# Kernel tuning notes

Measured on AMD Instinct MI355X. Metric: run time of the kernel, lower is better.

The kernel has to match this reference:

```python
import jax, jax.numpy as jnp
import numpy as np

D_MODEL = 768
H = 12
D_FF = 3072
EPS = 1e-6


def _layernorm(x, alpha, bias):
    # torch.std default is Bessel-corrected (ddof=1); denom is (std + eps)
    mean = jnp.mean(x, axis=-1, keepdims=True)
    var = jnp.sum((x - mean) ** 2, axis=-1, keepdims=True) / (x.shape[-1] - 1)
    std = jnp.sqrt(var)
    return alpha * (x - mean) / (std + EPS) + bias


def _linear(x, w, b):
    # torch nn.Linear: y = x @ W.T + b, W is [out, in]
    return jnp.einsum('...i,oi->...o', x, w) + b


def setup_inputs() -> dict:
    key = jax.random.key(0)
    ks = jax.random.split(key, 16)
    B, S = 8, 1024
    sc = 1.0 / np.sqrt(D_MODEL)
    inp = {
        'x': jax.random.normal(ks[0], (B, S, D_MODEL), dtype=jnp.float32),
        'mask': jax.random.randint(ks[1], (B, 1, 1, S), 0, 2, dtype=jnp.int32),
        'wq': jax.random.normal(ks[2], (D_MODEL, D_MODEL), dtype=jnp.float32) * sc,
        'bq': jnp.zeros((D_MODEL,), jnp.float32),
        'wk': jax.random.normal(ks[3], (D_MODEL, D_MODEL), dtype=jnp.float32) * sc,
        'bk': jnp.zeros((D_MODEL,), jnp.float32),
        'wv': jax.random.normal(ks[4], (D_MODEL, D_MODEL), dtype=jnp.float32) * sc,
        'bv': jnp.zeros((D_MODEL,), jnp.float32),
        'wo': jax.random.normal(ks[5], (D_MODEL, D_MODEL), dtype=jnp.float32) * sc,
        'bo': jnp.zeros((D_MODEL,), jnp.float32),
        'ln1_a': jnp.ones((D_MODEL,), jnp.float32),
        'ln1_b': jnp.zeros((D_MODEL,), jnp.float32),
        'ln2_a': jnp.ones((D_MODEL,), jnp.float32),
        'ln2_b': jnp.zeros((D_MODEL,), jnp.float32),
        'w1': jax.random.normal(ks[6], (D_FF, D_MODEL), dtype=jnp.float32) * sc,
        'b1': jnp.zeros((D_FF,), jnp.float32),
        'w2': jax.random.normal(ks[7], (D_MODEL, D_FF), dtype=jnp.float32) * (1.0 / np.sqrt(D_FF)),
        'b2': jnp.zeros((D_MODEL,), jnp.float32),
    }
    return inp


def reference(x, mask, wq, bq, wk, bk, wv, bv, wo, bo,
              ln1_a, ln1_b, ln2_a, ln2_b, w1, b1, w2, b2):
    B, S, _ = x.shape
    d_k = D_MODEL // H

    # --- residual 1: pre-LN self-attention (dropout identity at eval) ---
    xn = _layernorm(x, ln1_a, ln1_b)
    q = _linear(xn, wq, bq).reshape(B, S, H, d_k).transpose(0, 2, 1, 3)
    k = _linear(xn, wk, bk).reshape(B, S, H, d_k).transpose(0, 2, 1, 3)
    v = _linear(xn, wv, bv).reshape(B, S, H, d_k).transpose(0, 2, 1, 3)

    scores = jnp.einsum('bhqd,bhkd->bhqk', q, k) / jnp.sqrt(jnp.float32(d_k))
    # faithful quirk: masked positions set to 1e-9, NOT -inf
    scores = jnp.where(mask == 0, jnp.float32(1e-9), scores)
    attn = jax.nn.softmax(scores, axis=-1)
    ctx = jnp.einsum('bhqk,bhkd->bhqd', attn, v)
    ctx = ctx.transpose(0, 2, 1, 3).reshape(B, S, D_MODEL)
    x = x + _linear(ctx, wo, bo)

    # --- residual 2: pre-LN feed-forward ---
    xn = _layernorm(x, ln2_a, ln2_b)
    ff = _linear(jax.nn.relu(_linear(xn, w1, b1)), w2, b2)
    return x + ff
```

## Files before the change

### kernel.cpp

```cpp
#include <hip/hip_runtime.h>
#include <stdint.h>

#define D_MODEL 768
#define D_FF    3072
#define NH      12
#define DK      64
#define BB      8
#define SS      1024
#define NTOK    (BB*SS)
#define QST     2304

typedef float          f32x4  __attribute__((ext_vector_type(4)));
typedef __bf16         bf16x8 __attribute__((ext_vector_type(8)));
typedef unsigned short us8v   __attribute__((ext_vector_type(8)));
typedef unsigned short us4v   __attribute__((ext_vector_type(4)));

__device__ __forceinline__ unsigned short f2b(float f) {
  unsigned int u = __builtin_bit_cast(unsigned int, f);
  u = (u + 0x7fffu + ((u >> 16) & 1u)) >> 16;
  return (unsigned short)u;
}
__device__ __forceinline__ float b2f(unsigned short h) {
  unsigned int u = ((unsigned int)h) << 16;
  return __builtin_bit_cast(float, u);
}
__device__ __forceinline__ float exp2a(float x) {
  float r; asm("v_exp_f32 %0, %1" : "=v"(r) : "v"(x)); return r;
}
__device__ __forceinline__ unsigned int cvtpk(float lo, float hi) {
  unsigned int r;
  asm("v_cvt_pk_bf16_f32 %0, %1, %2" : "=v"(r) : "v"(lo), "v"(hi));
  return r;
}

#define N4TOT 1769472
__global__ __launch_bounds__(256) void cast6_kernel(
    const float* __restrict__ s0, const float* __restrict__ s1,
    const float* __restrict__ s2, const float* __restrict__ s3,
    const float* __restrict__ s4, const float* __restrict__ s5,
    unsigned short* __restrict__ d0, unsigned short* __restrict__ d1,
    unsigned short* __restrict__ d2, unsigned short* __restrict__ d3,
    unsigned short* __restrict__ d4, unsigned short* __restrict__ d5) {
  int i = blockIdx.x * 256 + threadIdx.x;
  if (i >= N4TOT) return;
  const float* src; unsigned short* dst; int off;
  if (i < 147456)       { src = s0; dst = d0; off = i; }
  else if (i < 294912)  { src = s1; dst = d1; off = i - 147456; }
  else if (i < 442368)  { src = s2; dst = d2; off = i - 294912; }
  else if (i < 589824)  { src = s3; dst = d3; off = i - 442368; }
  else if (i < 1179648) { src = s4; dst = d4; off = i - 589824; }
  else                  { src = s5; dst = d5; off = i - 1179648; }
  float4 f = ((const float4*)src)[off];
  us4v o; o.x = f2b(f.x); o.y = f2b(f.y); o.z = f2b(f.z); o.w = f2b(f.w);
  *(us4v*)(dst + (size_t)off * 4) = o;
}

__global__ __launch_bounds__(256) void ln_kernel(const float* __restrict__ x,
                                                 const float* __restrict__ ga,
                                                 const float* __restrict__ gb,
                                                 unsigned short* __restrict__ y) {
  int row = blockIdx.x;
  const float* xr = x + (size_t)row * D_MODEL;
  int t = threadIdx.x, w = t >> 6, l = t & 63;
  float v0 = xr[t], v1 = xr[t + 256], v2 = xr[t + 512];
  float s = v0 + v1 + v2;
  #pragma unroll
  for (int off = 32; off; off >>= 1) s += __shfl_xor(s, off);
  __shared__ float red[4];
  __shared__ float stats[2];
  if (l == 0) red[w] = s;
  __syncthreads();
  if (t == 0) stats[0] = (red[0] + red[1] + red[2] + red[3]) * (1.0f / 768.0f);
  __syncthreads();
  float mean = stats[0];
  float d0 = v0 - mean, d1 = v1 - mean, d2 = v2 - mean;
  float ss = d0 * d0 + d1 * d1 + d2 * d2;
  #pragma unroll
  for (int off = 32; off; off >>= 1) ss += __shfl_xor(ss, off);
  __syncthreads();
  if (l == 0) red[w] = ss;
  __syncthreads();
  if (t == 0) {
    float tot = red[0] + red[1] + red[2] + red[3];
    stats[1] = 1.0f / (sqrtf(tot * (1.0f / 767.0f)) + 1e-6f);
  }
  __syncthreads();
  float inv = stats[1];
  unsigned short* yr = y + (size_t)row * D_MODEL;
  yr[t]       = f2b(ga[t]       * (d0 * inv) + gb[t]);
  yr[t + 256] = f2b(ga[t + 256] * (d1 * inv) + gb[t + 256]);
  yr[t + 512] = f2b(ga[t + 512] * (d2 * inv) + gb[t + 512]);
}

#define GLDS(g, l) __builtin_amdgcn_global_load_lds( \
    (__attribute__((address_space(1))) const void*)(g), \
    (__attribute__((address_space(3))) void*)(l), 16, 0, 0)

template<int BN>
__global__ __launch_bounds__(256) void gemm_t(
    const unsigned short* __restrict__ A,
    const unsigned short* __restrict__ W,
    const float* __restrict__ biasA,
    const float* __restrict__ biasB,
    const float* __restrict__ biasC,
    int segw,
    const float* __restrict__ resid,
    float* __restrict__ outF,
    unsigned short* __restrict__ outB,
    int M, int N, int K, int relu) {
  constexpr int BK  = (BN == 128) ? 32 : 64;
  constexpr int WC  = (BN == 128) ? 2 : 1;
  constexpr int MF  = (BN == 128) ? 4 : 2;
  constexpr int NF  = 4;
  constexpr int ASZ = 128 * BK;
  constexpr int BSZ = BN * BK;
  __shared__ unsigned short As[2 * ASZ];
  __shared__ unsigned short Bs[2 * BSZ];
  int t = threadIdx.x;
  int w = t >> 6, l = t & 63;
  int brow = blockIdx.x * 128;
  int bcol = blockIdx.y * BN;
  int wr = (w / WC) * (MF * 16);
  int wc = (w % WC) * (NF * 16);

  const unsigned short *ga0, *ga1, *gb0, *gb1;
  if constexpr (BN == 128) {
    ga0 = A + (size_t)(brow + (t >> 2)) * K + (t & 3) * 8;
    ga1 = ga0 + (size_t)64 * K;
    gb0 = W + (size_t)(bcol + (t >> 2)) * K + (t & 3) * 8;
    gb1 = gb0 + (size_t)64 * K;
  } else {
    int r5 = t >> 3;
    int swz = (t & 7) ^ (r5 & 7);
    ga0 = A + (size_t)(brow + r5) * K + swz * 8;
    gb0 = W + (size_t)(bcol + r5) * K + swz * 8;
    ga1 = gb1 = nullptr;
  }

  f32x4 acc[MF][NF];
  #pragma unroll
  for (int m = 0; m < MF; m++)
    #pragma unroll
    for (int n = 0; n < NF; n++)
      acc[m][n] = (f32x4){0.f, 0.f, 0.f, 0.f};

  int arow = wr + (l & 15);
  int bcw  = wc + (l & 15);
  int g    = l >> 4;
  int kk   = g * 8;
  const int nt = K / BK;

  auto stage = [&](int ti, int buf) {
    int k0 = ti * BK;
    if constexpr (BN == 128) {
      GLDS(ga0 + k0, As + buf * ASZ + t * 8);
      GLDS(ga1 + k0, As + buf * ASZ + 2048 + t * 8);
      GLDS(gb0 + k0, Bs + buf * BSZ + t * 8);
      GLDS(gb1 + k0, Bs + buf * BSZ + 2048 + t * 8);
    } else {
      #pragma unroll
      for (int i = 0; i < 4; i++)
        GLDS(ga0 + k0 + (size_t)(32 * i) * K, As + buf * ASZ + i * 2048 + t * 8);
      #pragma unroll
      for (int i = 0; i < 2; i++)
        GLDS(gb0 + k0 + (size_t)(32 * i) * K, Bs + buf * BSZ + i * 2048 + t * 8);
    }
  };

  stage(0, 0);
  __syncthreads();

  int cb = 0;
  for (int ti = 0; ti < nt; ti++) {
    if (ti + 1 < nt) stage(ti + 1, cb ^ 1);
    #pragma unroll
    for (int h = 0; h < BK / 32; h++) {
      bf16x8 af[MF], bfv[NF];
      #pragma unroll
      for (int m = 0; m < MF; m++) {
        int aro = arow + m * 16;
        if constexpr (BN == 128)
          af[m] = *(const bf16x8*)(As + cb * ASZ + aro * 32 + kk);
        else
          af[m] = *(const bf16x8*)(As + cb * ASZ + aro * 64 +
                                   ((((h << 2) + g) ^ (l & 7)) << 3));
      }
      #pragma unroll
      for (int n = 0; n < NF; n++) {
        int bco = bcw + n * 16;
        if constexpr (BN == 128)
          bfv[n] = *(const bf16x8*)(Bs + cb * BSZ + bco * 32 + kk);
        else
          bfv[n] = *(const bf16x8*)(Bs + cb * BSZ + bco * 64 +
                                    ((((h << 2) + g) ^ (l & 7)) << 3));
      }
      #pragma unroll
      for (int m = 0; m < MF; m++)
        #pragma unroll
        for (int n = 0; n < NF; n++)
          acc[m][n] = __builtin_amdgcn_mfma_f32_16x16x32_bf16(af[m], bfv[n], acc[m][n], 0, 0, 0);
    }
    if (ti + 1 < nt) __syncthreads();
    cb ^= 1;
  }

  #pragma unroll
  for (int n = 0; n < NF; n++) {
    int col = bcol + wc + n * 16 + (l & 15);
    int seg = col / segw, off = col - seg * segw;
    const float* bp = (seg == 0) ? biasA : ((seg == 1) ? biasB : biasC);
    float bv = bp[off];
    #pragma unroll
    for (int m = 0; m < MF; m++) {
      int row0 = brow + wr + m * 16 + (l >> 4) * 4;
      #pragma unroll
      for (int r = 0; r < 4; r++) {
        int row = row0 + r;
        float vacc = acc[m][n][r] + bv;
        if (resid) vacc += resid[(size_t)row * N + col];
        if (relu)  vacc = fmaxf(vacc, 0.f);
        if (outF)  outF[(size_t)row * N + col] = vacc;
        if (outB)  outB[(size_t)row * N + col] = f2b(vacc);
      }
    }
  }
}

#define PPAD 72
#define KPAD 72
#define SM_C1 0.18033688011112043f

__global__ __launch_bounds__(256) void attn_mfma(
    const unsigned short* __restrict__ qkv,
    const int* __restrict__ mask,
    unsigned short* __restrict__ ctx) {
  int bh = blockIdx.x;
  int qt = blockIdx.y;
  int b = bh / NH, h = bh % NH;
  int t = threadIdx.x, w = t >> 6, l = t & 63;
  int ql = l & 15, g = l >> 4;

  const unsigned short* kp = qkv + 768 + h * DK;
  const unsigned short* vp = qkv + 1536 + h * DK;

  __shared__ unsigned short Ks[4096];
  __shared__ unsigned short Vt[64 * KPAD];
  __shared__ unsigned short Ps[128 * PPAD];
  __shared__ float mk01[64];
  __shared__ float lrw[4][2][16];

  int srow = t >> 3;
  int sblk = t & 7;
  int sb0  = sblk ^ (srow & 7);
  int sb1  = sblk ^ ((srow + 32) & 7);

  bf16x8 qf[2][2];
  {
    const unsigned short* qp = qkv + h * DK;
    size_t row0 = (size_t)(b * SS + qt * 128 + w * 32 + ql);
    #pragma unroll
    for (int s = 0; s < 2; s++)
      #pragma unroll
      for (int ks = 0; ks < 2; ks++)
        qf[s][ks] = *(const bf16x8*)(qp + (row0 + s * 16) * QST + ks * 32 + g * 8);
  }

  f32x4 acc_o[2][4];
  #pragma unroll
  for (int s = 0; s < 2; s++)
    #pragma unroll
    for (int nf = 0; nf < 4; nf++) acc_o[s][nf] = (f32x4){0.f, 0.f, 0.f, 0.f};
  float lrun[2] = {0.f, 0.f};

  for (int kt = 0; kt < 16; kt++) {
    size_t tok0 = (size_t)(b * SS + kt * 64);
    GLDS(kp + (tok0 + srow)      * QST + sb0 * 8, Ks + t * 8);
    GLDS(kp + (tok0 + srow + 32) * QST + sb1 * 8, Ks + 2048 + t * 8);
    {
      const unsigned short* vsrc = vp + (tok0 + l) * QST + w * 16;
      us8v v0 = *(const us8v*)vsrc;
      us8v v1 = *(const us8v*)(vsrc + 8);
      #pragma unroll
      for (int j = 0; j < 8; j++) {
        Vt[(w * 16 + j)     * KPAD + l] = v0[j];
        Vt[(w * 16 + 8 + j) * KPAD + l] = v1[j];
      }
    }
    if (t < 64) mk01[t] = mask[b * SS + kt * 64 + t] ? SM_C1 : 0.0f;
    __syncthreads();

    f32x4 sa[2][4];
    #pragma unroll
    for (int s = 0; s < 2; s++)
      #pragma unroll
      for (int kf = 0; kf < 4; kf++) sa[s][kf] = (f32x4){0.f, 0.f, 0.f, 0.f};
    #pragma unroll
    for (int ks = 0; ks < 2; ks++) {
      bf16x8 kfr[4];
      #pragma unroll
      for (int kf = 0; kf < 4; kf++) {
        int row = kf * 16 + ql;
        kfr[kf] = *(const bf16x8*)(Ks + row * 64 + ((g + 4 * ks) ^ (ql & 7)) * 8);
      }
      #pragma unroll
      for (int s = 0; s < 2; s++)
        #pragma unroll
        for (int kf = 0; kf < 4; kf++)
          sa[s][kf] = __builtin_amdgcn_mfma_f32_16x16x32_bf16(kfr[kf], qf[s][ks], sa[s][kf], 0, 0, 0);
    }

    float mv[16];
    #pragma unroll
    for (int kf = 0; kf < 4; kf++)
      #pragma unroll
      for (int r = 0; r < 4; r++)
        mv[kf * 4 + r] = mk01[kf * 16 + g * 4 + r];

    #pragma unroll
    for (int s = 0; s < 2; s++) {
      float pv[16];
      float rs = 0.f;
      #pragma unroll
      for (int i = 0; i < 16; i++) {
        pv[i] = exp2a(sa[s][i >> 2][i & 3] * mv[i]);
        rs += pv[i];
      }
      rs += __shfl_xor(rs, 16);
      rs += __shfl_xor(rs, 32);
      lrun[s] += rs;

      int prow = w * 32 + s * 16 + ql;
      #pragma unroll
      for (int kf = 0; kf < 4; kf++) {
        uint2 pk;
        pk.x = cvtpk(pv[kf * 4 + 0], pv[kf * 4 + 1]);
        pk.y = cvtpk(pv[kf * 4 + 2], pv[kf * 4 + 3]);
        *(uint2*)(Ps + prow * PPAD + kf * 16 + g * 4) = pk;
      }
    }

    #pragma unroll
    for (int ks = 0; ks < 2; ks++) {
      bf16x8 vfr[4];
      #pragma unroll
      for (int nf = 0; nf < 4; nf++)
        vfr[nf] = *(const bf16x8*)(Vt + (ql + nf * 16) * KPAD + g * 8 + ks * 32);
      #pragma unroll
      for (int s = 0; s < 2; s++) {
        bf16x8 pa = *(const bf16x8*)(Ps + (w * 32 + s * 16 + ql) * PPAD + g * 8 + ks * 32);
        #pragma unroll
        for (int nf = 0; nf < 4; nf++)
          acc_o[s][nf] = __builtin_amdgcn_mfma_f32_16x16x32_bf16(pa, vfr[nf], acc_o[s][nf], 0, 0, 0);
      }
    }
    __syncthreads();
  }

  #pragma unroll
  for (int s = 0; s < 2; s++)
    if (l < 16) lrw[w][s][l] = lrun[s];
  #pragma unroll
  for (int s = 0; s < 2; s++) {
    float li0 = 1.0f / lrw[w][s][g * 4 + 0], li1 = 1.0f / lrw[w][s][g * 4 + 1];
    float li2 = 1.0f / lrw[w][s][g * 4 + 2], li3 = 1.0f / lrw[w][s][g * 4 + 3];
    #pragma unroll
    for (int nf = 0; nf < 4; nf++) {
      #pragma unroll
      for (int r = 0; r < 4; r++) {
        float li = (r == 0) ? li0 : (r == 1) ? li1 : (r == 2) ? li2 : li3;
        int tok = b * SS + qt * 128 + w * 32 + s * 16 + g * 4 + r;
        ctx[(size_t)tok * D_MODEL + h * DK + nf * 16 + ql] = f2b(acc_o[s][nf][r] * li);
      }
    }
  }
}

extern "C" void kernel_launch(void* const* d_in, const int* in_sizes, int n_in,
                              void* d_out, int out_size, void* d_ws, size_t ws_size,
                              hipStream_t stream) {
  const float* x    = (const float*)d_in[0];
  const int*   mask = (const int*)d_in[1];
  const float* wq   = (const float*)d_in[2];
  const float* bq   = (const float*)d_in[3];
  const float* wk   = (const float*)d_in[4];
  const float* bk   = (const float*)d_in[5];
  const float* wv   = (const float*)d_in[6];
  const float* bv   = (const float*)d_in[7];
  const float* wo   = (const float*)d_in[8];
  const float* bo   = (const float*)d_in[9];
  const float* ln1a = (const float*)d_in[10];
  const float* ln1b = (const float*)d_in[11];
  const float* ln2a = (const float*)d_in[12];
  const float* ln2b = (const float*)d_in[13];
  const float* w1   = (const float*)d_in[14];
  const float* b1   = (const float*)d_in[15];
  const float* w2   = (const float*)d_in[16];
  const float* b2   = (const float*)d_in[17];

  char* ws = (char*)d_ws;
  unsigned short* wqkvb = (unsigned short*)(ws + 0);
  unsigned short* wob   = (unsigned short*)(ws + 3538944);
  unsigned short* w1b   = (unsigned short*)(ws + 4718592);
  unsigned short* w2b   = (unsigned short*)(ws + 9437184);
  unsigned short* xnb   = (unsigned short*)(ws + 14155776);
  unsigned short* qkvb  = (unsigned short*)(ws + 26738688);
  unsigned short* ctxb  = (unsigned short*)(ws + 64487424);
  float*          x1    = (float*)(ws + 26738688);
  unsigned short* h1b   = (unsigned short*)(ws + 51904512);

  cast6_kernel<<<N4TOT / 256, 256, 0, stream>>>(
      wq, wk, wv, wo, w1, w2,
      wqkvb, wqkvb + 589824, wqkvb + 1179648, wob, w1b, w2b);

  ln_kernel<<<NTOK, 256, 0, stream>>>(x, ln1a, ln1b, xnb);

  dim3 gqkv(NTOK / 128, QST / 64);
  gemm_t<64><<<gqkv, 256, 0, stream>>>(xnb, wqkvb, bq, bk, bv, 768,
                                       nullptr, nullptr, qkvb,
                                       NTOK, QST, D_MODEL, 0);

  dim3 ga(BB * NH, SS / 128);
  attn_mfma<<<ga, 256, 0, stream>>>(qkvb, mask, ctxb);

  dim3 gwo(NTOK / 128, D_MODEL / 64);
  gemm_t<64><<<gwo, 256, 0, stream>>>(ctxb, wob, bo, nullptr, nullptr, D_MODEL,
                                      x, x1, nullptr,
                                      NTOK, D_MODEL, D_MODEL, 0);

  ln_kernel<<<NTOK, 256, 0, stream>>>(x1, ln2a, ln2b, xnb);

  dim3 gff(NTOK / 128, D_FF / 64);
  gemm_t<64><<<gff, 256, 0, stream>>>(xnb, w1b, b1, nullptr, nullptr, D_FF,
                                      nullptr, nullptr, h1b,
                                      NTOK, D_FF, D_MODEL, 1);

  dim3 gff2(NTOK / 128, D_MODEL / 64);
  gemm_t<64><<<gff2, 256, 0, stream>>>(h1b, w2b, b2, nullptr, nullptr, D_MODEL,
                                       x1, (float*)d_out, nullptr,
                                       NTOK, D_MODEL, D_FF, 0);
}
```

Before: 263.5 us.

## Load GEMM A fragments directly from global into registers, skip LDS staging

The GEMM no longer stages the A tile in shared memory. Each wave loads its own 32-row A fragments straight from global memory into registers, double-buffered one K-tile ahead. Only the W tile still goes through LDS via global_load_lds. Since each wave owns distinct A rows, the intent is to halve LDS footprint and traffic and raise occupancy. The cost is more VGPR pressure and global A loads whose latency must now be hidden by the register prefetch.

```diff
diff --git a/kernel.cpp b/kernel.cpp
--- a/kernel.cpp
+++ b/kernel.cpp
@@ -96,8 +96,7 @@
     (__attribute__((address_space(1))) const void*)(g), \
     (__attribute__((address_space(3))) void*)(l), 16, 0, 0)
 
-template<int BN>
-__global__ __launch_bounds__(256) void gemm_t(
+__global__ __launch_bounds__(256) void gemm64(
     const unsigned short* __restrict__ A,
     const unsigned short* __restrict__ W,
     const float* __restrict__ biasA,
@@ -108,34 +107,24 @@
     float* __restrict__ outF,
     unsigned short* __restrict__ outB,
     int M, int N, int K, int relu) {
-  constexpr int BK  = (BN == 128) ? 32 : 64;
-  constexpr int WC  = (BN == 128) ? 2 : 1;
-  constexpr int MF  = (BN == 128) ? 4 : 2;
+  constexpr int BK  = 64;
+  constexpr int MF  = 2;
   constexpr int NF  = 4;
-  constexpr int ASZ = 128 * BK;
-  constexpr int BSZ = BN * BK;
-  __shared__ unsigned short As[2 * ASZ];
+  constexpr int BSZ = 64 * BK;
   __shared__ unsigned short Bs[2 * BSZ];
   int t = threadIdx.x;
   int w = t >> 6, l = t & 63;
   int brow = blockIdx.x * 128;
-  int bcol = blockIdx.y * BN;
-  int wr = (w / WC) * (MF * 16);
-  int wc = (w % WC) * (NF * 16);
-
-  const unsigned short *ga0, *ga1, *gb0, *gb1;
-  if constexpr (BN == 128) {
-    ga0 = A + (size_t)(brow + (t >> 2)) * K + (t & 3) * 8;
-    ga1 = ga0 + (size_t)64 * K;
-    gb0 = W + (size_t)(bcol + (t >> 2)) * K + (t & 3) * 8;
-    gb1 = gb0 + (size_t)64 * K;
-  } else {
-    int r5 = t >> 3;
-    int swz = (t & 7) ^ (r5 & 7);
-    ga0 = A + (size_t)(brow + r5) * K + swz * 8;
-    gb0 = W + (size_t)(bcol + r5) * K + swz * 8;
-    ga1 = gb1 = nullptr;
-  }
+  int bcol = blockIdx.y * 64;
+  int wr = w * 32;
+  int ql = l & 15, g = l >> 4;
+
+  int r5  = t >> 3;
+  int swz = (t & 7) ^ (r5 & 7);
+  const unsigned short* gb0 = W + (size_t)(bcol + r5) * K + swz * 8;
+
+  const unsigned short* ga0 = A + (size_t)(brow + wr + ql) * K + g * 8;
+  const unsigned short* ga1 = ga0 + (size_t)16 * K;
 
   f32x4 acc[MF][NF];
   #pragma unroll
@@ -144,75 +133,65 @@
     for (int n = 0; n < NF; n++)
       acc[m][n] = (f32x4){0.f, 0.f, 0.f, 0.f};
 
-  int arow = wr + (l & 15);
-  int bcw  = wc + (l & 15);
-  int g    = l >> 4;
-  int kk   = g * 8;
   const int nt = K / BK;
 
-  auto stage = [&](int ti, int buf) {
+  auto stageB = [&](int ti, int buf) {
     int k0 = ti * BK;
-    if constexpr (BN == 128) {
-      GLDS(ga0 + k0, As + buf * ASZ + t * 8);
-      GLDS(ga1 + k0, As + buf * ASZ + 2048 + t * 8);
-      GLDS(gb0 + k0, Bs + buf * BSZ + t * 8);
-      GLDS(gb1 + k0, Bs + buf * BSZ + 2048 + t * 8);
-    } else {
-      #pragma unroll
-      for (int i = 0; i < 4; i++)
-        GLDS(ga0 + k0 + (size_t)(32 * i) * K, As + buf * ASZ + i * 2048 + t * 8);
-      #pragma unroll
-      for (int i = 0; i < 2; i++)
-        GLDS(gb0 + k0 + (size_t)(32 * i) * K, Bs + buf * BSZ + i * 2048 + t * 8);
-    }
+    #pragma unroll
+    for (int i = 0; i < 2; i++)
+      GLDS(gb0 + k0 + (size_t)(32 * i) * K, Bs + buf * BSZ + i * 2048 + t * 8);
   };
 
-  stage(0, 0);
+  bf16x8 acur[MF][2], anxt[MF][2];
+  auto loadA = [&](int ti, bf16x8 dst[MF][2]) {
+    int k0 = ti * BK;
+    #pragma unroll
+    for (int h = 0; h < 2; h++) {
+      dst[0][h] = *(const bf16x8*)(ga0 + k0 + h * 32);
+      dst[1][h] = *(const bf16x8*)(ga1 + k0 + h * 32);
+    }
+  };
+
+  stageB(0, 0);
+  loadA(0, acur);
   __syncthreads();
 
   int cb = 0;
   for (int ti = 0; ti < nt; ti++) {
-    if (ti + 1 < nt) stage(ti + 1, cb ^ 1);
-    #pragma unroll
-    for (int h = 0; h < BK / 32; h++) {
-      bf16x8 af[MF], bfv[NF];
-      #pragma unroll
-      for (int m = 0; m < MF; m++) {
-        int aro = arow + m * 16;
-        if constexpr (BN == 128)
-          af[m] = *(const bf16x8*)(As + cb * ASZ + aro * 32 + kk);
-        else
-          af[m] = *(const bf16x8*)(As + cb * ASZ + aro * 64 +
-                                   ((((h << 2) + g) ^ (l & 7)) << 3));
-      }
-      #pragma unroll
-      for (int n = 0; n < NF; n++) {
-        int bco = bcw + n * 16;
-        if constexpr (BN == 128)
-          bfv[n] = *(const bf16x8*)(Bs + cb * BSZ + bco * 32 + kk);
-        else
-          bfv[n] = *(const bf16x8*)(Bs + cb * BSZ + bco * 64 +
-                                    ((((h << 2) + g) ^ (l & 7)) << 3));
-      }
+    if (ti + 1 < nt) { stageB(ti + 1, cb ^ 1); loadA(ti + 1, anxt); }
+    #pragma unroll
+    for (int h = 0; h < 2; h++) {
+      bf16x8 bfv[NF];
+      #pragma unroll
+      for (int n = 0; n < NF; n++)
+        bfv[n] = *(const bf16x8*)(Bs + cb * BSZ + (n * 16 + ql) * 64 +
+                                  ((((h << 2) + g) ^ (l & 7)) << 3));
       #pragma unroll
       for (int m = 0; m < MF; m++)
         #pragma unroll
         for (int n = 0; n < NF; n++)
-          acc[m][n] = __builtin_amdgcn_mfma_f32_16x16x32_bf16(af[m], bfv[n], acc[m][n], 0, 0, 0);
-    }
-    if (ti + 1 < nt) __syncthreads();
+          acc[m][n] = __builtin_amdgcn_mfma_f32_16x16x32_bf16(acur[m][h], bfv[n], acc[m][n], 0, 0, 0);
+    }
+    if (ti + 1 < nt) {
+      __syncthreads();
+      #pragma unroll
+      for (int m = 0; m < MF; m++)
+        #pragma unroll
+        for (int h = 0; h < 2; h++)
+          acur[m][h] = anxt[m][h];
+    }
     cb ^= 1;
   }
 
   #pragma unroll
   for (int n = 0; n < NF; n++) {
-    int col = bcol + wc + n * 16 + (l & 15);
+    int col = bcol + n * 16 + ql;
     int seg = col / segw, off = col - seg * segw;
     const float* bp = (seg == 0) ? biasA : ((seg == 1) ? biasB : biasC);
     float bv = bp[off];
     #pragma unroll
     for (int m = 0; m < MF; m++) {
-      int row0 = brow + wr + m * 16 + (l >> 4) * 4;
+      int row0 = brow + wr + m * 16 + g * 4;
       #pragma unroll
       for (int r = 0; r < 4; r++) {
         int row = row0 + r;
@@ -415,27 +394,27 @@
   ln_kernel<<<NTOK, 256, 0, stream>>>(x, ln1a, ln1b, xnb);
 
   dim3 gqkv(NTOK / 128, QST / 64);
-  gemm_t<64><<<gqkv, 256, 0, stream>>>(xnb, wqkvb, bq, bk, bv, 768,
-                                       nullptr, nullptr, qkvb,
-                                       NTOK, QST, D_MODEL, 0);
+  gemm64<<<gqkv, 256, 0, stream>>>(xnb, wqkvb, bq, bk, bv, 768,
+                                   nullptr, nullptr, qkvb,
+                                   NTOK, QST, D_MODEL, 0);
 
   dim3 ga(BB * NH, SS / 128);
   attn_mfma<<<ga, 256, 0, stream>>>(qkvb, mask, ctxb);
 
   dim3 gwo(NTOK / 128, D_MODEL / 64);
-  gemm_t<64><<<gwo, 256, 0, stream>>>(ctxb, wob, bo, nullptr, nullptr, D_MODEL,
-                                      x, x1, nullptr,
-                                      NTOK, D_MODEL, D_MODEL, 0);
+  gemm64<<<gwo, 256, 0, stream>>>(ctxb, wob, bo, nullptr, nullptr, D_MODEL,
+                                  x, x1, nullptr,
+                                  NTOK, D_MODEL, D_MODEL, 0);
 
   ln_kernel<<<NTOK, 256, 0, stream>>>(x1, ln2a, ln2b, xnb);
 
   dim3 gff(NTOK / 128, D_FF / 64);
-  gemm_t<64><<<gff, 256, 0, stream>>>(xnb, w1b, b1, nullptr, nullptr, D_FF,
-                                      nullptr, nullptr, h1b,
-                                      NTOK, D_FF, D_MODEL, 1);
+  gemm64<<<gff, 256, 0, stream>>>(xnb, w1b, b1, nullptr, nullptr, D_FF,
+                                  nullptr, nullptr, h1b,
+                                  NTOK, D_FF, D_MODEL, 1);
 
   dim3 gff2(NTOK / 128, D_MODEL / 64);
-  gemm_t<64><<<gff2, 256, 0, stream>>>(h1b, w2b, b2, nullptr, nullptr, D_MODEL,
-                                       x1, (float*)d_out, nullptr,
-                                       NTOK, D_MODEL, D_FF, 0);
-}
+  gemm64<<<gff2, 256, 0, stream>>>(h1b, w2b, b2, nullptr, nullptr, D_MODEL,
+                                   x1, (float*)d_out, nullptr,
+                                   NTOK, D_MODEL, D_FF, 0);
+}
```

Result: slower. 346.0 us (+31.3%).
